# Kernel optimization log

Measured on AMD Instinct MI355X. Metric: run time of the kernel, lower is better.

Reference implementation:

```python
import jax, jax.numpy as jnp
import numpy as np
import math

FACTOR = 5

def setup_inputs() -> dict:
    key = jax.random.key(0)
    k1, k2, k3, k4 = jax.random.split(key, 4)
    B, L, H, D = 4, 2048, 8, 64
    sample_k = FACTOR * math.ceil(math.log(L))  # 40
    queries = jax.random.normal(k1, (B, L, H, D), dtype=jnp.float32)
    keys = jax.random.normal(k2, (B, L, H, D), dtype=jnp.float32)
    values = jax.random.normal(k3, (B, L, H, D), dtype=jnp.float32)
    index_sample = jax.random.randint(k4, (L, sample_k), 0, L, dtype=jnp.int32)
    return {"queries": queries, "keys": keys, "values": values, "index_sample": index_sample}

def reference(queries, keys, values, index_sample):
    B, L_Q, H, D = queries.shape
    L_K = keys.shape[1]
    # [B,L,H,D] -> [B,H,L,D]
    Q = jnp.swapaxes(queries, 1, 2)
    K = jnp.swapaxes(keys, 1, 2)
    # values are cumsum'ed along the length axis before attention
    Vc = jnp.cumsum(jnp.swapaxes(values, 1, 2), axis=-2)
    u = min(FACTOR * math.ceil(math.log(L_Q)), L_Q)  # n_top
    # --- _prob_QK ---
    # gather sampled keys per query position: [B,H,L_Q,sample_k,D]
    K_sample = K[:, :, index_sample, :]
    # sampled scores: [B,H,L_Q,sample_k]
    Q_K_sample = jnp.einsum('bhqd,bhqsd->bhqs', Q, K_sample)
    # sparsity measure M = max - mean(scaled by L_K)
    M = Q_K_sample.max(axis=-1) - Q_K_sample.sum(axis=-1) / L_K  # [B,H,L_Q]
    M_top = jax.lax.top_k(M, u)[1]  # [B,H,u] query indices
    # gather top queries: [B,H,u,D]
    Q_reduce = jnp.take_along_axis(Q, M_top[..., None], axis=2)
    # full scores for selected queries: [B,H,u,L_K]
    scores = jnp.einsum('bhud,bhkd->bhuk', Q_reduce, K)
    scale = 1.0 / math.sqrt(D)
    scores = scores * scale
    # mask_flag=False, output_attention=False -> plain softmax then matmul with cumsum'ed V
    attn = jax.nn.softmax(scores, axis=-1)
    context = jnp.einsum('bhuk,bhkd->bhud', attn, Vc)  # [B,H,u,D]
    return context
```

## Files before the change

kernel.cpp:

```cpp
#include <hip/hip_runtime.h>
#include <math.h>

#define B 4
#define L 2048
#define H 8
#define D 64
#define SK 40
#define U 40
#define JC 16
#define JCL (L / JC)
#define CSG 32

#define OFF_M     0
#define OFF_TOP   262144
#define OFF_PART  270336
#define OFF_CSUM  5513216
#define OFF_VSUM  5677056

__device__ __forceinline__ float dot4(float4 a, float4 b) {
    return fmaf(a.x, b.x, fmaf(a.y, b.y, fmaf(a.z, b.z, a.w * b.w)));
}

__global__ __launch_bounds__(256) void k_msamp(const float* __restrict__ Q,
                                               const float* __restrict__ K,
                                               const int* __restrict__ idx,
                                               float* __restrict__ M) {
    int g  = blockIdx.x & 7;
    int b  = g >> 1;
    int hh = g & 1;
    int t  = threadIdx.x;
    int wave = t >> 6;
    int lane = t & 63;
    int qp = lane >> 5;
    int hp = (lane >> 3) & 3;
    int c  = lane & 7;
    int h  = hh * 4 + hp;
    int q  = (blockIdx.x >> 3) * 8 + wave * 2 + qp;

    const float* qrow = Q + (size_t)((b * L + q) * H + h) * D + c * 8;
    float4 qa = *(const float4*)qrow;
    float4 qb = *(const float4*)(qrow + 4);

    int s1 = lane & 31;
    int v1 = idx[q * SK + s1];
    int s2 = 32 + s1; if (s2 > SK - 1) s2 = SK - 1;
    int v2 = idx[q * SK + s2];

    const float* kbase = K + (size_t)b * L * H * D + (size_t)h * D + c * 8;

    float vmax = -__builtin_inff();
    float vsum = 0.f;
#pragma unroll 8
    for (int s = 0; s < SK; ++s) {
        int kidx = (s < 32) ? __shfl(v1, qp * 32 + s, 64)
                            : __shfl(v2, qp * 32 + (s - 32), 64);
        const float* kp = kbase + (size_t)kidx * (H * D);
        float4 ka = *(const float4*)kp;
        float4 kb = *(const float4*)(kp + 4);
        float d8 = dot4(qa, ka) + dot4(qb, kb);
        d8 += __shfl_xor(d8, 1, 64);
        d8 += __shfl_xor(d8, 2, 64);
        d8 += __shfl_xor(d8, 4, 64);
        vmax = fmaxf(vmax, d8);
        vsum += d8;
    }
    if (c == 0) M[(size_t)(b * H + h) * L + q] = vmax - vsum * (1.0f / (float)L);
}

__global__ __launch_bounds__(256) void k_topk(const float* __restrict__ M,
                                              int* __restrict__ top) {
    __shared__ unsigned long long cand[L];
    __shared__ unsigned int bins[256];
    __shared__ unsigned int red[256];
    __shared__ int cnt2;

    int bh = blockIdx.x;
    int tid = threadIdx.x;
    const float* m = M + (size_t)bh * L;

    bins[tid] = 0;
    if (tid == 0) cnt2 = 0;

    const float4* m4 = (const float4*)(m + tid * 8);
    float4 fa = m4[0], fb = m4[1];
    float f8[8] = {fa.x, fa.y, fa.z, fa.w, fb.x, fb.y, fb.z, fb.w};
    unsigned int u8[8];
    unsigned int umin = 0xFFFFFFFFu, umax = 0u;
#pragma unroll
    for (int e = 0; e < 8; ++e) {
        unsigned int bits = __float_as_uint(f8[e]);
        unsigned int u = (bits & 0x80000000u) ? ~bits : (bits | 0x80000000u);
        u8[e] = u;
        umin = min(umin, u);
        umax = max(umax, u);
    }
    red[tid] = umin;
    __syncthreads();
    for (int s = 128; s; s >>= 1) {
        if (tid < s) red[tid] = min(red[tid], red[tid + s]);
        __syncthreads();
    }
    unsigned int kmin = red[0];
    __syncthreads();
    red[tid] = umax;
    __syncthreads();
    for (int s = 128; s; s >>= 1) {
        if (tid < s) red[tid] = max(red[tid], red[tid + s]);
        __syncthreads();
    }
    unsigned int kmax = red[0];
    __syncthreads();

    unsigned int range = kmax - kmin;
    if (range == 0u) {
        if (tid < U) top[bh * U + tid] = tid;
        return;
    }
    int hb = 31 - __clz(range);
    int shift = (hb > 7) ? (hb - 7) : 0;

#pragma unroll
    for (int e = 0; e < 8; ++e) {
        unsigned int bin = (u8[e] - kmin) >> shift;
        atomicAdd(&bins[bin], 1u);
    }
    __syncthreads();

    red[tid] = bins[tid];
    __syncthreads();
    for (int s = 1; s < 256; s <<= 1) {
        unsigned int add = (tid + s < 256) ? red[tid + s] : 0u;
        __syncthreads();
        red[tid] += add;
        __syncthreads();
    }
    int cnt = __syncthreads_count(red[tid] >= U);
    unsigned int t = (unsigned int)(cnt - 1);

#pragma unroll
    for (int e = 0; e < 8; ++e) {
        unsigned int u = u8[e];
        if (((u - kmin) >> shift) >= t) {
            int pos = atomicAdd(&cnt2, 1);
            int i = tid * 8 + e;
            cand[pos] = ((unsigned long long)u << 11) | (unsigned long long)(2047 - i);
        }
    }
    __syncthreads();
    int C = cnt2;

    for (int j = tid; j < C; j += 256) {
        unsigned long long kj = cand[j];
        int r = 0;
        for (int kk = 0; kk < C; ++kk) r += (cand[kk] > kj);
        if (r < U) top[bh * U + r] = 2047 - (int)(kj & 0x7FFull);
    }
}

__global__ __launch_bounds__(512, 4) void k_phAB(const float* __restrict__ Q,
                                                 const float* __restrict__ K,
                                                 const int* __restrict__ top,
                                                 const float* __restrict__ V,
                                                 float* __restrict__ part,
                                                 float* __restrict__ csum,
                                                 float* __restrict__ vsum) {
    __shared__ __align__(16) float4 sQ4[U * 16];
    __shared__ __align__(16) float sE[U * JCL];
    int tid = threadIdx.x;
    int bh = blockIdx.x >> 4;
    int jc = blockIdx.x & 15;
    int b = bh >> 3, h = bh & (H - 1);

    for (int i = tid; i < U * 16; i += 512) {
        int u = i >> 4, c = i & 15;
        int qidx = top[bh * U + u];
        sQ4[i] = *((const float4*)(Q + (size_t)((b * L + qidx) * H + h) * D) + c);
    }

    int ugrp   = tid >> 7;
    int colgrp = tid & 127;
    int col = jc * 128 + colgrp;

    const float4* kr = (const float4*)(K + (size_t)((b * L + col) * H + h) * D);
    float4 kv[16];
#pragma unroll
    for (int i = 0; i < 16; ++i) kv[i] = kr[i];
    __syncthreads();

    int cs = 2 * jc + (colgrp >> 6);
#pragma unroll
    for (int uu = 0; uu < 10; ++uu) {
        int u = ugrp * 10 + uu;
        float s = 0.f;
#pragma unroll
        for (int i = 0; i < 16; ++i) s += dot4(sQ4[u * 16 + i], kv[i]);
        float e = __expf(s * 0.125f);
        sE[u * JCL + colgrp] = e;
        float c0 = e;
#pragma unroll
        for (int o = 1; o < 64; o <<= 1) c0 += __shfl_xor(c0, o, 64);
        if ((colgrp & 63) == 0) csum[((size_t)bh * U + u) * CSG + cs] = c0;
    }
    __syncthreads();

    int w8   = tid >> 6;
    int lane = tid & 63;
    for (int r = 0; r < 5; ++r) {
        int u = w8 * 5 + r;
        float el = sE[u * JCL + lane];
        float eh = sE[u * JCL + 64 + lane];
        float sh = eh;
#pragma unroll
        for (int s = 1; s < 64; s <<= 1) {
            float o = __shfl_down(sh, s, 64);
            sh += (lane + s < 64) ? o : 0.f;
        }
        float th = __shfl(sh, 0, 64);
        float sl = el;
#pragma unroll
        for (int s = 1; s < 64; s <<= 1) {
            float o = __shfl_down(sl, s, 64);
            sl += (lane + s < 64) ? o : 0.f;
        }
        sE[u * JCL + lane]      = sl + th;
        sE[u * JCL + 64 + lane] = sh;
    }

    int j2 = lane >> 4;
    int d4 = lane & 15;

    float4 acc[5];
#pragma unroll
    for (int uu = 0; uu < 5; ++uu) acc[uu] = make_float4(0.f, 0.f, 0.f, 0.f);
    float4 vs = make_float4(0.f, 0.f, 0.f, 0.f);

    const float* Vb = V + (size_t)(b * L) * (H * D) + (size_t)h * D + d4 * 4;
#pragma unroll 4
    for (int it = 0; it < JCL / 4; ++it) {
        int j = it * 4 + j2;
        float4 v4 = *(const float4*)(Vb + (size_t)(jc * JCL + j) * (H * D));
        vs.x += v4.x; vs.y += v4.y; vs.z += v4.z; vs.w += v4.w;
#pragma unroll
        for (int uu = 0; uu < 5; ++uu) {
            float tj = sE[(w8 * 5 + uu) * JCL + j];
            acc[uu].x = fmaf(tj, v4.x, acc[uu].x);
            acc[uu].y = fmaf(tj, v4.y, acc[uu].y);
            acc[uu].z = fmaf(tj, v4.z, acc[uu].z);
            acc[uu].w = fmaf(tj, v4.w, acc[uu].w);
        }
    }

    float* po = part + ((size_t)jc * (B * H) + bh) * (U * D);
#pragma unroll
    for (int uu = 0; uu < 5; ++uu) {
        float4 a = acc[uu];
        a.x += __shfl_xor(a.x, 16, 64); a.y += __shfl_xor(a.y, 16, 64);
        a.z += __shfl_xor(a.z, 16, 64); a.w += __shfl_xor(a.w, 16, 64);
        a.x += __shfl_xor(a.x, 32, 64); a.y += __shfl_xor(a.y, 32, 64);
        a.z += __shfl_xor(a.z, 32, 64); a.w += __shfl_xor(a.w, 32, 64);
        if (j2 == 0) *(float4*)(po + (w8 * 5 + uu) * D + d4 * 4) = a;
    }
    if (w8 == 0) {
        vs.x += __shfl_xor(vs.x, 16, 64); vs.y += __shfl_xor(vs.y, 16, 64);
        vs.z += __shfl_xor(vs.z, 16, 64); vs.w += __shfl_xor(vs.w, 16, 64);
        vs.x += __shfl_xor(vs.x, 32, 64); vs.y += __shfl_xor(vs.y, 32, 64);
        vs.z += __shfl_xor(vs.z, 32, 64); vs.w += __shfl_xor(vs.w, 32, 64);
        if (j2 == 0)
            *(float4*)(vsum + ((size_t)bh * JC + jc) * D + d4 * 4) = vs;
    }
}

__global__ __launch_bounds__(256) void k_red(const float* __restrict__ part,
                                             const float* __restrict__ csum,
                                             const float* __restrict__ vsum,
                                             float* __restrict__ out) {
    __shared__ float sden[4];
    __shared__ float stw[4][JC];
    int o = blockIdx.x * 256 + threadIdx.x;
    int bh = o / (U * D);
    int rest = o - bh * (U * D);
    int u = rest >> 6;
    int d = rest & 63;
    int tid = threadIdx.x;
    int ubase = ((blockIdx.x * 256) % (U * D)) >> 6;

    if (tid < 128) {
        int ul = tid >> 5, cs = tid & 31;
        float v = csum[((size_t)bh * U + ubase + ul) * CSG + cs];
#pragma unroll
        for (int s = 1; s < 32; s <<= 1) {
            float ov = __shfl_down(v, s, 64);
            v += (cs + s < 32) ? ov : 0.f;
        }
        if (cs == 0) { sden[ul] = v; stw[ul][JC - 1] = 0.f; }
        if ((cs & 1) == 0 && cs >= 2) stw[ul][(cs >> 1) - 1] = v;
    }
    __syncthreads();

    int ul = u - ubase;
    float s = 0.f;
#pragma unroll
    for (int jc = 0; jc < JC; ++jc)
        s += part[(size_t)(jc * (B * H) + bh) * (U * D) + rest];
#pragma unroll
    for (int jc = 0; jc < JC; ++jc)
        s = fmaf(stw[ul][jc], vsum[((size_t)bh * JC + jc) * D + d], s);
    out[o] = s / sden[ul];
}

extern "C" void kernel_launch(void* const* d_in, const int* in_sizes, int n_in,
                              void* d_out, int out_size, void* d_ws, size_t ws_size,
                              hipStream_t stream) {
    const float* Q  = (const float*)d_in[0];
    const float* K  = (const float*)d_in[1];
    const float* V  = (const float*)d_in[2];
    const int* idx  = (const int*)d_in[3];
    float* out = (float*)d_out;

    float* M    = (float*)((char*)d_ws + OFF_M);
    int*   top  = (int*)  ((char*)d_ws + OFF_TOP);
    float* part = (float*)((char*)d_ws + OFF_PART);
    float* csum = (float*)((char*)d_ws + OFF_CSUM);
    float* vsum = (float*)((char*)d_ws + OFF_VSUM);

    k_msamp<<<(L / 8) * 8, 256, 0, stream>>>(Q, K, idx, M);
    k_topk<<<B * H, 256, 0, stream>>>(M, top);
    k_phAB<<<B * H * JC, 512, 0, stream>>>(Q, K, top, V, part, csum, vsum);
    k_red<<<(B * H * U * D) / 256, 256, 0, stream>>>(part, csum, vsum, out);
}
```

Before: 140.1 us.

## Bucket sampled key indices by chunk and compute sampled scores from LDS-tiled keys

A new kernel buckets each query's sampled key indices by 256-key chunk into a per-chunk edge list. The sampled-score kernel then stages a 256-row K tile in LDS for each (batch, head, chunk) and computes partial max and sum for every query from LDS rather than through scattered global gathers. The top-k kernel merges the per-chunk partials to form M. This adds an extra launch, a workspace round trip for edges and partials, divergent variable-length loops, and Q is reloaded by every chunk block.

```diff
diff --git a/kernel.cpp b/kernel.cpp
--- a/kernel.cpp
+++ b/kernel.cpp
@@ -10,64 +10,110 @@
 #define JC 16
 #define JCL (L / JC)
 #define CSG 32
-
-#define OFF_M     0
-#define OFF_TOP   262144
-#define OFF_PART  270336
-#define OFF_CSUM  5513216
-#define OFF_VSUM  5677056
+#define KCH 256
+#define NCH (L / KCH)
+#define ECAP 40
+
+#define OFF_PMAX  0
+#define OFF_PSUM  2097152
+#define OFF_CNT   4194304
+#define OFF_EDGE  4259840
+#define OFF_TOP   4915200
+#define OFF_PART  4920320
+#define OFF_CSUM  10163200
+#define OFF_VSUM  10327040
 
 __device__ __forceinline__ float dot4(float4 a, float4 b) {
     return fmaf(a.x, b.x, fmaf(a.y, b.y, fmaf(a.z, b.z, a.w * b.w)));
 }
 
-__global__ __launch_bounds__(256) void k_msamp(const float* __restrict__ Q,
-                                               const float* __restrict__ K,
-                                               const int* __restrict__ idx,
-                                               float* __restrict__ M) {
-    int g  = blockIdx.x & 7;
-    int b  = g >> 1;
-    int hh = g & 1;
-    int t  = threadIdx.x;
-    int wave = t >> 6;
-    int lane = t & 63;
-    int qp = lane >> 5;
-    int hp = (lane >> 3) & 3;
-    int c  = lane & 7;
-    int h  = hh * 4 + hp;
-    int q  = (blockIdx.x >> 3) * 8 + wave * 2 + qp;
-
-    const float* qrow = Q + (size_t)((b * L + q) * H + h) * D + c * 8;
-    float4 qa = *(const float4*)qrow;
-    float4 qb = *(const float4*)(qrow + 4);
-
-    int s1 = lane & 31;
-    int v1 = idx[q * SK + s1];
-    int s2 = 32 + s1; if (s2 > SK - 1) s2 = SK - 1;
-    int v2 = idx[q * SK + s2];
-
-    const float* kbase = K + (size_t)b * L * H * D + (size_t)h * D + c * 8;
-
-    float vmax = -__builtin_inff();
-    float vsum = 0.f;
-#pragma unroll 8
+__global__ __launch_bounds__(512) void k_build(const int* __restrict__ idx,
+                                               unsigned char* __restrict__ edges,
+                                               int* __restrict__ cnts) {
+    int c = blockIdx.x >> 2;
+    int q = (blockIdx.x & 3) * 512 + threadIdx.x;
+
+    int v[SK];
+#pragma unroll
+    for (int j = 0; j < SK / 4; ++j) {
+        int4 t = *(const int4*)(idx + q * SK + j * 4);
+        v[j * 4 + 0] = t.x; v[j * 4 + 1] = t.y;
+        v[j * 4 + 2] = t.z; v[j * 4 + 3] = t.w;
+    }
+    unsigned char* ep = edges + (size_t)(c * L + q) * ECAP;
+    int cnt = 0;
+#pragma unroll
     for (int s = 0; s < SK; ++s) {
-        int kidx = (s < 32) ? __shfl(v1, qp * 32 + s, 64)
-                            : __shfl(v2, qp * 32 + (s - 32), 64);
-        const float* kp = kbase + (size_t)kidx * (H * D);
-        float4 ka = *(const float4*)kp;
-        float4 kb = *(const float4*)(kp + 4);
-        float d8 = dot4(qa, ka) + dot4(qb, kb);
-        d8 += __shfl_xor(d8, 1, 64);
-        d8 += __shfl_xor(d8, 2, 64);
-        d8 += __shfl_xor(d8, 4, 64);
-        vmax = fmaxf(vmax, d8);
-        vsum += d8;
-    }
-    if (c == 0) M[(size_t)(b * H + h) * L + q] = vmax - vsum * (1.0f / (float)L);
-}
-
-__global__ __launch_bounds__(256) void k_topk(const float* __restrict__ M,
+        if ((v[s] >> 8) == c) ep[cnt++] = (unsigned char)(v[s] & 255);
+    }
+    cnts[c * L + q] = cnt;
+}
+
+__global__ __launch_bounds__(512, 4) void k_msamp2(const float* __restrict__ Q,
+                                                   const float* __restrict__ K,
+                                                   const unsigned char* __restrict__ edges,
+                                                   const int* __restrict__ cnts,
+                                                   float* __restrict__ pmax,
+                                                   float* __restrict__ psum) {
+    __shared__ __align__(16) float sK[KCH * 68];
+    int bid = blockIdx.x;
+    int qh = bid & 1;
+    int kc = (bid >> 1) & 7;
+    int bh = bid >> 4;
+    int b = bh >> 3, h = bh & (H - 1);
+    int tid = threadIdx.x;
+
+#pragma unroll
+    for (int p = 0; p < 8; ++p) {
+        int row = p * 32 + (tid >> 4);
+        int c16 = tid & 15;
+        const float4* src = (const float4*)(K +
+            (size_t)((b * L + kc * KCH + row) * H + h) * D + c16 * 4);
+        *(float4*)&sK[row * 68 + c16 * 4] = *src;
+    }
+    __syncthreads();
+
+    int g = tid >> 3;
+    int c = tid & 7;
+
+    for (int batch = 0; batch < 16; ++batch) {
+        int q = qh * 1024 + batch * 64 + g;
+        const float* qrow = Q + (size_t)((b * L + q) * H + h) * D + c * 8;
+        float4 qa = *(const float4*)qrow;
+        float4 qb = *(const float4*)(qrow + 4);
+
+        int cnt = cnts[kc * L + q];
+        const unsigned char* ep = edges + (size_t)(kc * L + q) * ECAP;
+
+        float vmax = -__builtin_inff();
+        float vsum = 0.f;
+        for (int eb = 0; eb < cnt; eb += 4) {
+            unsigned int u4 = *(const unsigned int*)(ep + eb);
+#pragma unroll
+            for (int j = 0; j < 4; ++j) {
+                if (eb + j < cnt) {
+                    int r = (u4 >> (8 * j)) & 255;
+                    const float* kp = &sK[r * 68 + c * 8];
+                    float4 ka = *(const float4*)kp;
+                    float4 kb = *(const float4*)(kp + 4);
+                    float d8 = dot4(qa, ka) + dot4(qb, kb);
+                    d8 += __shfl_xor(d8, 1, 64);
+                    d8 += __shfl_xor(d8, 2, 64);
+                    d8 += __shfl_xor(d8, 4, 64);
+                    vmax = fmaxf(vmax, d8);
+                    vsum += d8;
+                }
+            }
+        }
+        if (c == 0) {
+            pmax[(size_t)(bh * NCH + kc) * L + q] = vmax;
+            psum[(size_t)(bh * NCH + kc) * L + q] = vsum;
+        }
+    }
+}
+
+__global__ __launch_bounds__(256) void k_topk(const float* __restrict__ pmax,
+                                              const float* __restrict__ psum,
                                               int* __restrict__ top) {
     __shared__ unsigned long long cand[L];
     __shared__ unsigned int bins[256];
@@ -76,14 +122,24 @@
 
     int bh = blockIdx.x;
     int tid = threadIdx.x;
-    const float* m = M + (size_t)bh * L;
 
     bins[tid] = 0;
     if (tid == 0) cnt2 = 0;
 
-    const float4* m4 = (const float4*)(m + tid * 8);
-    float4 fa = m4[0], fb = m4[1];
-    float f8[8] = {fa.x, fa.y, fa.z, fa.w, fb.x, fb.y, fb.z, fb.w};
+    float f8[8];
+#pragma unroll
+    for (int e = 0; e < 8; ++e) {
+        int q = tid * 8 + e;
+        float mx = pmax[(size_t)(bh * NCH) * L + q];
+        float sm = psum[(size_t)(bh * NCH) * L + q];
+#pragma unroll
+        for (int cc = 1; cc < NCH; ++cc) {
+            mx = fmaxf(mx, pmax[(size_t)(bh * NCH + cc) * L + q]);
+            sm += psum[(size_t)(bh * NCH + cc) * L + q];
+        }
+        f8[e] = mx - sm * (1.0f / (float)L);
+    }
+
     unsigned int u8[8];
     unsigned int umin = 0xFFFFFFFFu, umax = 0u;
 #pragma unroll
@@ -317,14 +373,18 @@
     const int* idx  = (const int*)d_in[3];
     float* out = (float*)d_out;
 
-    float* M    = (float*)((char*)d_ws + OFF_M);
+    float* pmax = (float*)((char*)d_ws + OFF_PMAX);
+    float* psum = (float*)((char*)d_ws + OFF_PSUM);
+    int*   cnts = (int*)  ((char*)d_ws + OFF_CNT);
+    unsigned char* edges = (unsigned char*)((char*)d_ws + OFF_EDGE);
     int*   top  = (int*)  ((char*)d_ws + OFF_TOP);
     float* part = (float*)((char*)d_ws + OFF_PART);
     float* csum = (float*)((char*)d_ws + OFF_CSUM);
     float* vsum = (float*)((char*)d_ws + OFF_VSUM);
 
-    k_msamp<<<(L / 8) * 8, 256, 0, stream>>>(Q, K, idx, M);
-    k_topk<<<B * H, 256, 0, stream>>>(M, top);
+    k_build<<<NCH * 4, 512, 0, stream>>>(idx, edges, cnts);
+    k_msamp2<<<B * H * NCH * 2, 512, 0, stream>>>(Q, K, edges, cnts, pmax, psum);
+    k_topk<<<B * H, 256, 0, stream>>>(pmax, psum, top);
     k_phAB<<<B * H * JC, 512, 0, stream>>>(Q, K, top, V, part, csum, vsum);
     k_red<<<(B * H * U * D) / 256, 256, 0, stream>>>(part, csum, vsum, out);
 }
```

Result: slower. 167.5 us (+19.5%).
